# Kernel tuning notes

Hardware: AMD Instinct MI355X
Metric: run time of the kernel (lower is better)

## Reference

```python
import jax, jax.numpy as jnp
import numpy as np

C, H, W = 256, 512, 512
K = 32768  # number of changed input pixels


def setup_inputs() -> dict:
    key = jax.random.key(0)
    k1, k2, k3 = jax.random.split(key, 3)
    inp = jax.random.normal(k1, (1, C, H, W), dtype=jnp.float32)
    # persistent output state from previous frame (floor mode: OH=H//2, OW=W//2)
    state = jax.random.normal(k2, (1, C, H // 2, W // 2), dtype=jnp.float32)
    change = jax.random.randint(k3, (K,), 0, H * W, dtype=jnp.int32)
    return {"input": inp, "outputState": state, "changeIndexes": change}


def reference(input, outputState, changeIndexes):
    # changeIndexes are flat spatial indices (y*W + x) of changed input pixels.
    # Each changed pixel maps to output pixel (y//2, x//2); recompute the 2x2
    # max over all channels and scatter into the persistent outputState.
    _, c, h, w = input.shape
    y = changeIndexes // w          # [K]
    x = changeIndexes % w           # [K]
    oy = y // 2                     # [K] output row
    ox = x // 2                     # [K] output col
    iy = oy * 2                     # top-left of 2x2 window
    ix = ox * 2
    # gather the 4 window elements for every changed pixel: each [C, K]
    v = jnp.maximum(
        jnp.maximum(input[0, :, iy, ix], input[0, :, iy, ix + 1]),
        jnp.maximum(input[0, :, iy + 1, ix], input[0, :, iy + 1, ix + 1]),
    )
    # scatter recomputed pooled values into state (duplicates write same value)
    out = outputState.at[0, :, oy, ox].set(v)
    return out
```

## Files before the change

kernel.cpp:

```cpp
#include <hip/hip_runtime.h>

#define C_  256
#define H_  512
#define W_  512
#define OH_ 256
#define OW_ 256

typedef float f4 __attribute__((ext_vector_type(4)));

__device__ __forceinline__ f4 ntload4(const float* p) {
    return __builtin_nontemporal_load(reinterpret_cast<const f4*>(p));
}
__device__ __forceinline__ void ntstore4(float* p, f4 v) {
    __builtin_nontemporal_store(v, reinterpret_cast<f4*>(p));
}

__global__ void cbpool_set_mask(const int* __restrict__ change, int K,
                                unsigned int* __restrict__ mask) {
    int k = blockIdx.x * blockDim.x + threadIdx.x;
    if (k >= K) return;
    int idx = change[k];
    int y = idx >> 9;
    int x = idx & (W_ - 1);
    int bit = (y >> 1) * OW_ + (x >> 1);
    atomicOr(&mask[bit >> 5], 1u << (bit & 31));
}

__global__ void __launch_bounds__(256)
cbpool_fused(const float* __restrict__ in,
             const float* __restrict__ state,
             const unsigned int* __restrict__ mask,
             float* __restrict__ out) {
    int tid = blockIdx.x * blockDim.x + threadIdx.x;
    int q  = tid & 63;
    int oy = (tid >> 6) & (OH_ - 1);
    int c  = tid >> 14;

    const float* inrow = in + ((size_t)c << 18) + ((size_t)oy << 10) + (q << 3);
    f4 a0 = ntload4(inrow);
    f4 a1 = ntload4(inrow + 4);
    f4 b0 = ntload4(inrow + W_);
    f4 b1 = ntload4(inrow + W_ + 4);

    f4 pooled;
    pooled.x = fmaxf(fmaxf(a0.x, a0.y), fmaxf(b0.x, b0.y));
    pooled.y = fmaxf(fmaxf(a0.z, a0.w), fmaxf(b0.z, b0.w));
    pooled.z = fmaxf(fmaxf(a1.x, a1.y), fmaxf(b1.x, b1.y));
    pooled.w = fmaxf(fmaxf(a1.z, a1.w), fmaxf(b1.z, b1.w));

    size_t obase = ((size_t)c << 16) + (oy << 8) + (q << 2);
    f4 s = ntload4(state + obase);

    unsigned int m = mask[(oy << 3) + (q >> 3)];
    int sh = (q << 2) & 31;

    f4 o;
    o.x = ((m >> (sh + 0)) & 1u) ? pooled.x : s.x;
    o.y = ((m >> (sh + 1)) & 1u) ? pooled.y : s.y;
    o.z = ((m >> (sh + 2)) & 1u) ? pooled.z : s.z;
    o.w = ((m >> (sh + 3)) & 1u) ? pooled.w : s.w;
    ntstore4(out + obase, o);
}

extern "C" void kernel_launch(void* const* d_in, const int* in_sizes, int n_in,
                              void* d_out, int out_size, void* d_ws, size_t ws_size,
                              hipStream_t stream) {
    const float* in     = (const float*)d_in[0];
    const float* state  = (const float*)d_in[1];
    const int*   change = (const int*)d_in[2];
    float*       out    = (float*)d_out;
    unsigned int* mask  = (unsigned int*)d_ws;

    const int K = in_sizes[2];

    hipMemsetAsync(mask, 0, (OH_ * OW_ / 32) * sizeof(unsigned int), stream);
    cbpool_set_mask<<<(K + 255) / 256, 256, 0, stream>>>(change, K, mask);

    const int total_quads = C_ * OH_ * (OW_ / 4);
    cbpool_fused<<<total_quads / 256, 256, 0, stream>>>(in, state, mask, out);
}
```

Baseline: 76.51 us.

## Build mask in one LDS block and process two output rows per thread

Replaces the memset plus global-atomic mask kernel with a single-block kernel that builds the 8 KB bitmask in shared memory and copies it out, removing a launch and the global atomics. The main streaming kernel now has each thread handle two output rows, giving more loads in flight per thread and half as many threads. The single-block mask build serializes 32K shared atomics on one CU and assumes K is a multiple of 4, since any tail elements are dropped.

Result: no change. 77.69 us (+1.5%).

```diff
diff --git a/kernel.cpp b/kernel.cpp
--- a/kernel.cpp
+++ b/kernel.cpp
@@ -15,15 +15,28 @@
     __builtin_nontemporal_store(v, reinterpret_cast<f4*>(p));
 }
 
-__global__ void cbpool_set_mask(const int* __restrict__ change, int K,
-                                unsigned int* __restrict__ mask) {
-    int k = blockIdx.x * blockDim.x + threadIdx.x;
-    if (k >= K) return;
-    int idx = change[k];
-    int y = idx >> 9;
-    int x = idx & (W_ - 1);
-    int bit = (y >> 1) * OW_ + (x >> 1);
-    atomicOr(&mask[bit >> 5], 1u << (bit & 31));
+__global__ void __launch_bounds__(256)
+cbpool_build_mask(const int* __restrict__ change, int K,
+                  unsigned int* __restrict__ mask) {
+    __shared__ unsigned int lmask[OH_ * OW_ / 32];
+    for (int i = threadIdx.x; i < OH_ * OW_ / 32; i += 256)
+        lmask[i] = 0u;
+    __syncthreads();
+    const int4* c4 = reinterpret_cast<const int4*>(change);
+    for (int k = threadIdx.x; k < K / 4; k += 256) {
+        int4 v = c4[k];
+        #pragma unroll
+        for (int j = 0; j < 4; ++j) {
+            int idx = (j == 0) ? v.x : (j == 1) ? v.y : (j == 2) ? v.z : v.w;
+            int y = idx >> 9;
+            int x = idx & (W_ - 1);
+            int bit = (y >> 1) * OW_ + (x >> 1);
+            atomicOr(&lmask[bit >> 5], 1u << (bit & 31));
+        }
+    }
+    __syncthreads();
+    for (int i = threadIdx.x; i < OH_ * OW_ / 32; i += 256)
+        mask[i] = lmask[i];
 }
 
 __global__ void __launch_bounds__(256)
@@ -32,34 +45,51 @@
              const unsigned int* __restrict__ mask,
              float* __restrict__ out) {
     int tid = blockIdx.x * blockDim.x + threadIdx.x;
-    int q  = tid & 63;
-    int oy = (tid >> 6) & (OH_ - 1);
-    int c  = tid >> 14;
+    int q   = tid & 63;
+    int oyp = (tid >> 6) & 127;
+    int c   = tid >> 13;
 
-    const float* inrow = in + ((size_t)c << 18) + ((size_t)oy << 10) + (q << 3);
-    f4 a0 = ntload4(inrow);
-    f4 a1 = ntload4(inrow + 4);
-    f4 b0 = ntload4(inrow + W_);
-    f4 b1 = ntload4(inrow + W_ + 4);
+    const float* ib = in + ((size_t)c << 18) + ((size_t)oyp << 11) + (q << 3);
+    f4 L0a = ntload4(ib);
+    f4 L0b = ntload4(ib + 4);
+    f4 L1a = ntload4(ib + W_);
+    f4 L1b = ntload4(ib + W_ + 4);
+    f4 L2a = ntload4(ib + 2 * W_);
+    f4 L2b = ntload4(ib + 2 * W_ + 4);
+    f4 L3a = ntload4(ib + 3 * W_);
+    f4 L3b = ntload4(ib + 3 * W_ + 4);
 
-    f4 pooled;
-    pooled.x = fmaxf(fmaxf(a0.x, a0.y), fmaxf(b0.x, b0.y));
-    pooled.y = fmaxf(fmaxf(a0.z, a0.w), fmaxf(b0.z, b0.w));
-    pooled.z = fmaxf(fmaxf(a1.x, a1.y), fmaxf(b1.x, b1.y));
-    pooled.w = fmaxf(fmaxf(a1.z, a1.w), fmaxf(b1.z, b1.w));
+    size_t ob = ((size_t)c << 16) + ((size_t)oyp << 9) + (q << 2);
+    f4 s0 = ntload4(state + ob);
+    f4 s1 = ntload4(state + ob + OW_);
 
-    size_t obase = ((size_t)c << 16) + (oy << 8) + (q << 2);
-    f4 s = ntload4(state + obase);
-
-    unsigned int m = mask[(oy << 3) + (q >> 3)];
+    int mw = (oyp << 4) + (q >> 3);
+    unsigned int m0 = mask[mw];
+    unsigned int m1 = mask[mw + 8];
     int sh = (q << 2) & 31;
 
-    f4 o;
-    o.x = ((m >> (sh + 0)) & 1u) ? pooled.x : s.x;
-    o.y = ((m >> (sh + 1)) & 1u) ? pooled.y : s.y;
-    o.z = ((m >> (sh + 2)) & 1u) ? pooled.z : s.z;
-    o.w = ((m >> (sh + 3)) & 1u) ? pooled.w : s.w;
-    ntstore4(out + obase, o);
+    f4 p0, p1;
+    p0.x = fmaxf(fmaxf(L0a.x, L0a.y), fmaxf(L1a.x, L1a.y));
+    p0.y = fmaxf(fmaxf(L0a.z, L0a.w), fmaxf(L1a.z, L1a.w));
+    p0.z = fmaxf(fmaxf(L0b.x, L0b.y), fmaxf(L1b.x, L1b.y));
+    p0.w = fmaxf(fmaxf(L0b.z, L0b.w), fmaxf(L1b.z, L1b.w));
+    p1.x = fmaxf(fmaxf(L2a.x, L2a.y), fmaxf(L3a.x, L3a.y));
+    p1.y = fmaxf(fmaxf(L2a.z, L2a.w), fmaxf(L3a.z, L3a.w));
+    p1.z = fmaxf(fmaxf(L2b.x, L2b.y), fmaxf(L3b.x, L3b.y));
+    p1.w = fmaxf(fmaxf(L2b.z, L2b.w), fmaxf(L3b.z, L3b.w));
+
+    f4 o0, o1;
+    o0.x = ((m0 >> (sh + 0)) & 1u) ? p0.x : s0.x;
+    o0.y = ((m0 >> (sh + 1)) & 1u) ? p0.y : s0.y;
+    o0.z = ((m0 >> (sh + 2)) & 1u) ? p0.z : s0.z;
+    o0.w = ((m0 >> (sh + 3)) & 1u) ? p0.w : s0.w;
+    o1.x = ((m1 >> (sh + 0)) & 1u) ? p1.x : s1.x;
+    o1.y = ((m1 >> (sh + 1)) & 1u) ? p1.y : s1.y;
+    o1.z = ((m1 >> (sh + 2)) & 1u) ? p1.z : s1.z;
+    o1.w = ((m1 >> (sh + 3)) & 1u) ? p1.w : s1.w;
+
+    ntstore4(out + ob,       o0);
+    ntstore4(out + ob + OW_, o1);
 }
 
 extern "C" void kernel_launch(void* const* d_in, const int* in_sizes, int n_in,
@@ -73,9 +103,8 @@
 
     const int K = in_sizes[2];
 
-    hipMemsetAsync(mask, 0, (OH_ * OW_ / 32) * sizeof(unsigned int), stream);
-    cbpool_set_mask<<<(K + 255) / 256, 256, 0, stream>>>(change, K, mask);
+    cbpool_build_mask<<<1, 256, 0, stream>>>(change, K, mask);
 
-    const int total_quads = C_ * OH_ * (OW_ / 4);
-    cbpool_fused<<<total_quads / 256, 256, 0, stream>>>(in, state, mask, out);
+    const int total_threads = C_ * (OH_ / 2) * (OW_ / 4);
+    cbpool_fused<<<total_threads / 256, 256, 0, stream>>>(in, state, mask, out);
 }
```
